# Performance work log

Hardware: AMD Instinct MI355X
Metric: run time of the kernel (lower is better)

The kernel has to match this reference:

```python
import jax, jax.numpy as jnp
import numpy as np

B, N, C = 2, 2048, 1024
H, D = 16, 64  # n_q_heads, head_dim
EPS = 1e-6


def setup_inputs() -> dict:
    key = jax.random.key(0)
    ks = jax.random.split(key, 6)
    x = jax.random.normal(ks[0], (B, N, C), dtype=jnp.float32)
    context = jax.random.normal(ks[1], (B, N, C), dtype=jnp.float32)
    # realistic RoPE tables, rotary_dim = head_dim (non-interleaved GLM-style)
    inv_freq = 1.0 / (10000.0 ** (np.arange(0, D, 2, dtype=np.float32) / D))
    ang = np.arange(N, dtype=np.float32)[:, None] * inv_freq[None, :]  # [N, D/2]
    ang = np.concatenate([ang, ang], axis=-1)  # [N, D]
    cos = jnp.broadcast_to(jnp.cos(ang)[None], (B, N, D)).astype(jnp.float32)
    sin = jnp.broadcast_to(jnp.sin(ang)[None], (B, N, D)).astype(jnp.float32)
    s = 1.0 / np.sqrt(C)
    Wq = jax.random.normal(ks[2], (2 * C, C), dtype=jnp.float32) * s
    Wkv = jax.random.normal(ks[3], (2 * C, C), dtype=jnp.float32) * s
    Wo = jax.random.normal(ks[4], (C, C), dtype=jnp.float32) * s
    bo = jnp.zeros((C,), dtype=jnp.float32)
    q_norm_w = jnp.ones((D,), dtype=jnp.float32)
    k_norm_w = jnp.ones((D,), dtype=jnp.float32)
    return {"x": x, "context": context, "cos": cos, "sin": sin,
            "Wq": Wq, "Wkv": Wkv, "Wo": Wo, "bo": bo,
            "q_norm_w": q_norm_w, "k_norm_w": k_norm_w}


def _zm_rmsnorm(t, w):
    # zero-mean RMSNorm over last (head_dim) axis: LayerNorm without bias
    t = t - jnp.mean(t, axis=-1, keepdims=True)
    var = jnp.mean(t * t, axis=-1, keepdims=True)
    return t * jax.lax.rsqrt(var + EPS) * w


def _rotate_half(t):
    t1, t2 = jnp.split(t, 2, axis=-1)
    return jnp.concatenate([-t2, t1], axis=-1)


def reference(x, context, cos, sin, Wq, Wkv, Wo, bo, q_norm_w, k_norm_w):
    b, n1, c = x.shape
    n2 = context.shape[1]
    # fused q+gate projection: [b, n1, 2*C] -> [b, n1, H, 2D], per-head chunk
    qg = (x @ Wq.T).reshape(b, n1, H, 2 * D)
    q = qg[..., :D]                      # [b, n1, H, D]
    gate = qg[..., D:].reshape(b, n1, H * D)  # [b, n1, C]
    q = _zm_rmsnorm(q, q_norm_w).transpose(0, 2, 1, 3)  # [b, H, n1, D]
    # fused k+v projection: [b, n2, 2*C] -> [b, n2, H, 2D]
    kv = (context @ Wkv.T).reshape(b, n2, H, 2 * D)
    k = _zm_rmsnorm(kv[..., :D], k_norm_w).transpose(0, 2, 1, 3)  # [b, H, n2, D]
    v = kv[..., D:].transpose(0, 2, 1, 3)                         # [b, H, n2, D]
    # RoPE (full head_dim rotary)
    cos_b = cos[:, None]  # [b, 1, n, D]
    sin_b = sin[:, None]
    q = q * cos_b + _rotate_half(q) * sin_b
    k = k * cos_b + _rotate_half(k) * sin_b
    # SDPA (non-causal cross attention)
    scale = D ** -0.5
    scores = jnp.einsum('bhqd,bhkd->bhqk', q, k) * scale
    attn = jax.nn.softmax(scores, axis=-1)
    attn_out = jnp.einsum('bhqk,bhkd->bhqd', attn, v)
    attn_out = attn_out.transpose(0, 2, 1, 3).reshape(b, n1, H * D)  # [b, n1, C]
    # gated output combine + out projection
    attn_out = attn_out * jax.nn.sigmoid(gate)
    return attn_out @ Wo.T + bo
```

## Files before the change

### kernel.cpp

```cpp
#include <hip/hip_runtime.h>
#include <cstdint>
#include <cstddef>


#define B_ 2
#define N_ 2048
#define C_ 1024
#define H_ 16
#define D_ 64
#define K_ 1024
#define PK_ 2048
#define EPS_ 1e-6f
#define LOG2E_ 1.44269504088896f
#define SMAX_ 12.0f

typedef __bf16 b16x8 __attribute__((ext_vector_type(8)));
typedef float f32x4 __attribute__((ext_vector_type(4)));

__device__ __forceinline__ unsigned short f2bf(float f) {
  union { float f; unsigned u; } a; a.f = f;
  unsigned r = a.u + 0x7FFFu + ((a.u >> 16) & 1u);
  return (unsigned short)(r >> 16);
}
__device__ __forceinline__ float bf2f(unsigned short u) {
  union { unsigned u; float f; } a; a.u = ((unsigned)u) << 16; return a.f;
}

__device__ __forceinline__ void cast_one(const float* __restrict__ src,
                                         unsigned short* __restrict__ dst, int e) {
  float4 v = *(const float4*)(src + e);
  *(ushort4*)(dst + e) = make_ushort4(f2bf(v.x), f2bf(v.y), f2bf(v.z), f2bf(v.w));
}

__device__ __forceinline__ void pack_one(const float* __restrict__ src,
                                         unsigned short* __restrict__ dst, int e) {
  float4 v = *(const float4*)(src + e);
  const int r = e >> 10, k = e & 1023;
  unsigned short* p = dst + ((size_t)r << 11) + ((k >> 5) << 6) + (k & 31);
  const unsigned short h0 = f2bf(v.x), h1 = f2bf(v.y), h2 = f2bf(v.z), h3 = f2bf(v.w);
  *(ushort4*)p = make_ushort4(h0, h1, h2, h3);
  *(ushort4*)(p + 32) = make_ushort4(f2bf(v.x - bf2f(h0)), f2bf(v.y - bf2f(h1)),
                                     f2bf(v.z - bf2f(h2)), f2bf(v.w - bf2f(h3)));
}

__global__ __launch_bounds__(256) void pack_all(
    const float* __restrict__ x, const float* __restrict__ Wq,
    const float* __restrict__ ctx, const float* __restrict__ Wkv,
    const float* __restrict__ Wo,
    unsigned short* __restrict__ xb, unsigned short* __restrict__ wqb,
    unsigned short* __restrict__ cb, unsigned short* __restrict__ wkvb,
    unsigned short* __restrict__ wop)
{
  const int e = (blockIdx.x * 256 + threadIdx.x) << 2;
  if (e < 4194304)       cast_one(x,   xb,  e);
  else if (e < 6291456)  cast_one(Wq,  wqb, e - 4194304);
  else if (e < 10485760) cast_one(ctx, cb,  e - 6291456);
  else if (e < 12582912) cast_one(Wkv, wkvb, e - 10485760);
  else                   pack_one(Wo,  wop, e - 12582912);
}

__global__ __launch_bounds__(256) void gemm_qkv(
    const unsigned short* __restrict__ xb, const unsigned short* __restrict__ wqb,
    const unsigned short* __restrict__ cb, const unsigned short* __restrict__ wkvb,
    const float* __restrict__ cosb, const float* __restrict__ sinb,
    const float* __restrict__ qnw, const float* __restrict__ knw,
    unsigned short* __restrict__ Qbo, unsigned short* __restrict__ Kbo,
    unsigned short* __restrict__ gate, unsigned short* __restrict__ vt, float qscale)
{
  __shared__ __align__(16) unsigned short As[128 * 64];
  __shared__ __align__(16) unsigned short Bs[128 * 64];
  const int tid = threadIdx.x, lane = tid & 63, wave = tid >> 6;

  const int id = blockIdx.x;
  const int swz = (id & 7) * 128 + (id >> 3);
  const bool isQ = swz < 512;
  const int local = swz & 511;
  const int bm = (local >> 4) << 7, bn = (local & 15) << 7;
  const int wm = (wave >> 1) << 6, wn = (wave & 1) << 6;

  const unsigned short* Ap = isQ ? xb : cb;
  const unsigned short* Bp = isQ ? wqb : wkvb;

  const int srow = lane >> 3;
  const int sslot = (lane & 7) ^ srow;
  const size_t rbytes = (size_t)K_ * 2;
  const char* aSrc = (const char*)Ap + (size_t)(bm + srow) * rbytes + (sslot << 4);
  const char* bSrc = (const char*)Bp + (size_t)(bn + srow) * rbytes + (sslot << 4);

  f32x4 acc[4][4];
  #pragma unroll
  for (int i = 0; i < 4; ++i)
    #pragma unroll
    for (int j = 0; j < 4; ++j) acc[i][j] = (f32x4){0.f, 0.f, 0.f, 0.f};

  const int fr = lane & 15, fs = lane >> 4;

  for (int ks = 0; ks < K_ / 64; ++ks) {
    const size_t ko = (size_t)ks << 7;
    #pragma unroll
    for (int i = 0; i < 4; ++i) {
      const int g = (wave << 2) + i;
      __builtin_amdgcn_global_load_lds(
          (const __attribute__((address_space(1))) void*)(aSrc + (size_t)(g << 3) * rbytes + ko),
          (__attribute__((address_space(3))) void*)((char*)As + (g << 10)), 16, 0, 0);
      __builtin_amdgcn_global_load_lds(
          (const __attribute__((address_space(1))) void*)(bSrc + (size_t)(g << 3) * rbytes + ko),
          (__attribute__((address_space(3))) void*)((char*)Bs + (g << 10)), 16, 0, 0);
    }
    __syncthreads();

    b16x8 a[4][2], b[4][2];
    #pragma unroll
    for (int t = 0; t < 4; ++t) {
      const int ar = wm + (t << 4) + fr;
      const char* pa = (const char*)As + (ar << 7);
      a[t][0] = *(const b16x8*)(pa + ((fs ^ (ar & 7)) << 4));
      a[t][1] = *(const b16x8*)(pa + (((4 + fs) ^ (ar & 7)) << 4));
      const int br = wn + (t << 4) + fr;
      const char* pb = (const char*)Bs + (br << 7);
      b[t][0] = *(const b16x8*)(pb + ((fs ^ (br & 7)) << 4));
      b[t][1] = *(const b16x8*)(pb + (((4 + fs) ^ (br & 7)) << 4));
    }
    #pragma unroll
    for (int mi = 0; mi < 4; ++mi)
      #pragma unroll
      for (int ni = 0; ni < 4; ++ni) {
        acc[mi][ni] = __builtin_amdgcn_mfma_f32_16x16x32_bf16(a[mi][0], b[ni][0], acc[mi][ni], 0, 0, 0);
        acc[mi][ni] = __builtin_amdgcn_mfma_f32_16x16x32_bf16(a[mi][1], b[ni][1], acc[mi][ni], 0, 0, 0);
      }
    __syncthreads();
  }

  const int g = lane >> 4;
  const int h = bn >> 7;
  if (wn == 0) {
    const float* nw = isQ ? qnw : knw;
    const float oscale = isQ ? qscale : 1.0f;
    unsigned short* nOut = isQ ? Qbo : Kbo;
    float wv[4];
    #pragma unroll
    for (int ni = 0; ni < 4; ++ni) wv[ni] = nw[(ni << 4) + fr];
    #pragma unroll
    for (int mi = 0; mi < 4; ++mi) {
      #pragma unroll
      for (int r = 0; r < 4; ++r) {
        const int t = bm + wm + (mi << 4) + (g << 2) + r;
        float v0 = acc[mi][0][r], v1 = acc[mi][1][r];
        float v2 = acc[mi][2][r], v3 = acc[mi][3][r];
        float s = (v0 + v1) + (v2 + v3);
        #pragma unroll
        for (int off = 1; off < 16; off <<= 1) s += __shfl_xor(s, off);
        const float mean = s * (1.f / 64.f);
        v0 -= mean; v1 -= mean; v2 -= mean; v3 -= mean;
        float s2 = (v0*v0 + v1*v1) + (v2*v2 + v3*v3);
        #pragma unroll
        for (int off = 1; off < 16; off <<= 1) s2 += __shfl_xor(s2, off);
        const float rq = rsqrtf(s2 * (1.f / 64.f) + EPS_);
        const float x0 = v0 * rq * wv[0], x1 = v1 * rq * wv[1];
        const float x2 = v2 * rq * wv[2], x3 = v3 * rq * wv[3];
        const float* cr = cosb + (size_t)t * 64;
        const float* sr = sinb + (size_t)t * 64;
        const float o0 = x0 * cr[fr]    - x2 * sr[fr];
        const float o1 = x1 * cr[16+fr] - x3 * sr[16+fr];
        const float o2 = x2 * cr[32+fr] + x0 * sr[32+fr];
        const float o3 = x3 * cr[48+fr] + x1 * sr[48+fr];
        unsigned short* dp = nOut + (((size_t)((t >> 11) * H_ + h)) * N_ + (t & 2047)) * 64;
        dp[fr]      = f2bf(o0 * oscale);
        dp[16 + fr] = f2bf(o1 * oscale);
        dp[32 + fr] = f2bf(o2 * oscale);
        dp[48 + fr] = f2bf(o3 * oscale);
      }
    }
  } else if (isQ) {
    #pragma unroll
    for (int mi = 0; mi < 4; ++mi)
      #pragma unroll
      for (int r = 0; r < 4; ++r) {
        const int t = bm + wm + (mi << 4) + (g << 2) + r;
        unsigned short* gp = gate + (size_t)t * C_ + h * 64;
        #pragma unroll
        for (int ni = 0; ni < 4; ++ni) gp[(ni << 4) + fr] = f2bf(acc[mi][ni][r]);
      }
  } else {
    #pragma unroll
    for (int mi = 0; mi < 4; ++mi) {
      const int t0 = bm + wm + (mi << 4) + (g << 2);
      const int bb = t0 >> 11, n0 = t0 & 2047;
      #pragma unroll
      for (int ni = 0; ni < 4; ++ni) {
        const int dv = (ni << 4) + fr;
        ushort4 pk = make_ushort4(f2bf(acc[mi][ni][0]), f2bf(acc[mi][ni][1]),
                                  f2bf(acc[mi][ni][2]), f2bf(acc[mi][ni][3]));
        *(ushort4*)(vt + ((size_t)(bb * H_ + h) * 64 + dv) * N_ + n0) = pk;
      }
    }
  }
}

__global__ __launch_bounds__(256) void gemm_nt_hilo(
    const unsigned short* __restrict__ Ap, const unsigned short* __restrict__ Bp,
    float* __restrict__ Cm, int M, int N, const float* __restrict__ bias)
{
  __shared__ __align__(16) unsigned short As[128 * 64];
  __shared__ __align__(16) unsigned short Bs[64 * 64];
  const int tid = threadIdx.x, lane = tid & 63, wave = tid >> 6;

  const int nwg = gridDim.x, id = blockIdx.x;
  const int swz = (id & 7) * (nwg >> 3) + (id >> 3);
  const int nbn = N >> 6;
  const int bm = (swz / nbn) << 7, bn = (swz % nbn) << 6;
  const int wm = (wave >> 1) << 6, wn = (wave & 1) << 5;

  const int srow = lane >> 3;
  const int sslot = (lane & 7) ^ srow;
  const size_t rbytes = (size_t)K_ * 4;
  const char* aSrc = (const char*)Ap + (size_t)(bm + srow) * rbytes + (sslot << 4);
  const char* bSrc = (const char*)Bp + (size_t)(bn + srow) * rbytes + (sslot << 4);

  f32x4 acc[4][2];
  #pragma unroll
  for (int i = 0; i < 4; ++i)
    #pragma unroll
    for (int j = 0; j < 2; ++j) acc[i][j] = (f32x4){0.f, 0.f, 0.f, 0.f};

  const int fr = lane & 15, fs = lane >> 4;
  const int hoff = (fs ^ (fr & 7)) << 4;

  for (int ks = 0; ks < K_ / 32; ++ks) {
    const size_t ko = (size_t)ks << 7;
    #pragma unroll
    for (int i = 0; i < 4; ++i) {
      const int ga = (wave << 2) + i;
      __builtin_amdgcn_global_load_lds(
          (const __attribute__((address_space(1))) void*)(aSrc + (size_t)(ga << 3) * rbytes + ko),
          (__attribute__((address_space(3))) void*)((char*)As + (ga << 10)), 16, 0, 0);
    }
    #pragma unroll
    for (int i = 0; i < 2; ++i) {
      const int gb = (wave << 1) + i;
      __builtin_amdgcn_global_load_lds(
          (const __attribute__((address_space(1))) void*)(bSrc + (size_t)(gb << 3) * rbytes + ko),
          (__attribute__((address_space(3))) void*)((char*)Bs + (gb << 10)), 16, 0, 0);
    }
    __syncthreads();

    b16x8 ah[4], al[4], bh[2], bl[2];
    #pragma unroll
    for (int t = 0; t < 4; ++t) {
      const char* pa = (const char*)As + ((wm + (t << 4) + fr) << 7);
      ah[t] = *(const b16x8*)(pa + hoff);
      al[t] = *(const b16x8*)(pa + (hoff ^ 64));
    }
    #pragma unroll
    for (int t = 0; t < 2; ++t) {
      const char* pb = (const char*)Bs + ((wn + (t << 4) + fr) << 7);
      bh[t] = *(const b16x8*)(pb + hoff);
      bl[t] = *(const b16x8*)(pb + (hoff ^ 64));
    }
    #pragma unroll
    for (int mi = 0; mi < 4; ++mi)
      #pragma unroll
      for (int ni = 0; ni < 2; ++ni) {
        acc[mi][ni] = __builtin_amdgcn_mfma_f32_16x16x32_bf16(ah[mi], bh[ni], acc[mi][ni], 0, 0, 0);
        acc[mi][ni] = __builtin_amdgcn_mfma_f32_16x16x32_bf16(al[mi], bh[ni], acc[mi][ni], 0, 0, 0);
        acc[mi][ni] = __builtin_amdgcn_mfma_f32_16x16x32_bf16(ah[mi], bl[ni], acc[mi][ni], 0, 0, 0);
      }
    __syncthreads();
  }

  const int rbase = (lane >> 4) << 2;
  #pragma unroll
  for (int mi = 0; mi < 4; ++mi)
    #pragma unroll
    for (int ni = 0; ni < 2; ++ni) {
      const int n = bn + wn + (ni << 4) + fr;
      const float badd = bias ? bias[n] : 0.f;
      #pragma unroll
      for (int r = 0; r < 4; ++r) {
        const int m = bm + wm + (mi << 4) + rbase + r;
        Cm[(size_t)m * N + n] = acc[mi][ni][r] + badd;
      }
    }
}

__global__ __launch_bounds__(256) void flash_bf16(
    const unsigned short* __restrict__ Qb, const unsigned short* __restrict__ Kb,
    const unsigned short* __restrict__ Vt, const unsigned short* __restrict__ gateb,
    unsigned short* __restrict__ gp)
{
  const int id = blockIdx.x;
  const int swzb = (id & 7) * 64 + (id >> 3);
  const int q0 = (swzb & 15) * 128;
  const int h = (swzb >> 4) & 15;
  const int b = swzb >> 8;
  const int tid = threadIdx.x, lane = tid & 63, wave = tid >> 6;
  __shared__ __align__(16) unsigned short Ks[2][64 * 64];
  __shared__ __align__(16) unsigned short Vss[2][64 * 64];
  __shared__ __align__(16) __bf16 Ps[4][2][16][72];
  const int bh = b * H_ + h;
  const int g = lane >> 4, fr = lane & 15;

  b16x8 qA0, qA1, qB0, qB1;
  {
    const unsigned short* QrowA = Qb + ((size_t)bh * N_ + q0 + wave*32 + fr) * D_;
    qA0 = *(const b16x8*)(QrowA + (g << 3));
    qA1 = *(const b16x8*)(QrowA + 32 + (g << 3));
    qB0 = *(const b16x8*)(QrowA + 16 * D_ + (g << 3));
    qB1 = *(const b16x8*)(QrowA + 16 * D_ + 32 + (g << 3));
  }

  f32x4 oA[4], oB[4];
  #pragma unroll
  for (int r = 0; r < 4; ++r) {
    oA[r] = (f32x4){0.f, 0.f, 0.f, 0.f};
    oB[r] = (f32x4){0.f, 0.f, 0.f, 0.f};
  }
  float lA = 0.f, lB = 0.f;

  const unsigned short* Kbh  = Kb + (size_t)bh * N_ * D_;
  const unsigned short* Vtbh = Vt + (size_t)bh * D_ * N_;
  const int swzK = ((lane & 7) ^ (lane >> 3)) << 4;
  __bf16* PwA = &Ps[wave][0][0][0] + fr * 72;
  __bf16* PwB = &Ps[wave][1][0][0] + fr * 72;

  #define STAGE(buf, j0)                                                          \
    {                                                                             \
      _Pragma("unroll")                                                           \
      for (int i = 0; i < 2; ++i) {                                               \
        const int gg = wave * 2 + i;                                              \
        const char* ksrc = (const char*)(Kbh + (size_t)((j0) + gg * 8) * D_) +    \
                           (lane >> 3) * 128 + swzK;                              \
        __builtin_amdgcn_global_load_lds(                                         \
            (const __attribute__((address_space(1))) void*)ksrc,                  \
            (__attribute__((address_space(3))) void*)((char*)Ks[buf] + gg * 1024),\
            16, 0, 0);                                                            \
        const int dv = gg * 8 + (lane >> 3);                                      \
        const char* vsrc = (const char*)(Vtbh + (size_t)dv * N_ + (j0)) + swzK;   \
        __builtin_amdgcn_global_load_lds(                                         \
            (const __attribute__((address_space(1))) void*)vsrc,                  \
            (__attribute__((address_space(3))) void*)((char*)Vss[buf] + gg * 1024),\
            16, 0, 0);                                                            \
      }                                                                           \
    }

  STAGE(0, 0);
  int cur = 0;
  for (int j0 = 0; j0 < N_; j0 += 64) {
    __syncthreads();
    if (j0 + 64 < N_) STAGE(cur ^ 1, j0 + 64);

    const unsigned short* Kbuf = Ks[cur];
    const unsigned short* Vbuf = Vss[cur];
    const int cb0 = g << 4;
    __builtin_amdgcn_s_setprio(1);
    #pragma unroll
    for (int t = 0; t < 4; ++t) {
      const int krow = t * 16 + fr;
      const char* kbp = (const char*)Kbuf + krow * 128;
      const int f = (krow & 7) << 4;
      b16x8 kf0 = *(const b16x8*)(kbp + (cb0 ^ f));
      b16x8 kf1 = *(const b16x8*)(kbp + ((64 + cb0) ^ f));
      f32x4 sA = __builtin_amdgcn_mfma_f32_16x16x32_bf16(kf0, qA0, (f32x4){0.f,0.f,0.f,0.f}, 0, 0, 0);
      sA = __builtin_amdgcn_mfma_f32_16x16x32_bf16(kf1, qA1, sA, 0, 0, 0);
      f32x4 sB = __builtin_amdgcn_mfma_f32_16x16x32_bf16(kf0, qB0, (f32x4){0.f,0.f,0.f,0.f}, 0, 0, 0);
      sB = __builtin_amdgcn_mfma_f32_16x16x32_bf16(kf1, qB1, sB, 0, 0, 0);
      union { __bf16 hb[4]; ushort4 u4; } pkA, pkB;
      #pragma unroll
      for (int r = 0; r < 4; ++r) {
        const float pA = __builtin_amdgcn_exp2f(sA[r] - SMAX_);
        lA += pA;
        pkA.hb[r] = (__bf16)pA;
        const float pB = __builtin_amdgcn_exp2f(sB[r] - SMAX_);
        lB += pB;
        pkB.hb[r] = (__bf16)pB;
      }
      *(ushort4*)(PwA + t * 16 + (g << 2)) = pkA.u4;
      *(ushort4*)(PwB + t * 16 + (g << 2)) = pkB.u4;
    }
    __builtin_amdgcn_s_setprio(0);

    b16x8 pfA[2], pfB[2];
    #pragma unroll
    for (int c = 0; c < 2; ++c) {
      pfA[c] = *(const b16x8*)(PwA + c * 32 + (g << 3));
      pfB[c] = *(const b16x8*)(PwB + c * 32 + (g << 3));
    }

    __builtin_amdgcn_s_setprio(1);
    #pragma unroll
    for (int dt = 0; dt < 4; ++dt) {
      const int vrow = dt * 16 + fr;
      const char* vbp = (const char*)Vbuf + vrow * 128;
      const int fv = (vrow & 7) << 4;
      #pragma unroll
      for (int c = 0; c < 2; ++c) {
        b16x8 vf = *(const b16x8*)(vbp + ((c * 64 + cb0) ^ fv));
        oA[dt] = __builtin_amdgcn_mfma_f32_16x16x32_bf16(pfA[c], vf, oA[dt], 0, 0, 0);
        oB[dt] = __builtin_amdgcn_mfma_f32_16x16x32_bf16(pfB[c], vf, oB[dt], 0, 0, 0);
      }
    }
    __builtin_amdgcn_s_setprio(0);
    cur ^= 1;
  }
  #undef STAGE

  lA += __shfl_xor(lA, 16); lA += __shfl_xor(lA, 32);
  lB += __shfl_xor(lB, 16); lB += __shfl_xor(lB, 32);

  #pragma unroll
  for (int r = 0; r < 4; ++r) {
    const float lqA = __shfl(lA, (g << 2) + r);
    const float lqB = __shfl(lB, (g << 2) + r);
    #pragma unroll
    for (int set = 0; set < 2; ++set) {
      const float inv = 1.f / (set ? lqB : lqA);
      const int q = q0 + wave * 32 + set * 16 + (g << 2) + r;
      const size_t qa = (size_t)(b * N_ + q);
      #pragma unroll
      for (int dt = 0; dt < 4; ++dt) {
        const int d = (dt << 4) + fr;
        const float o = (set ? oB[dt][r] : oA[dt][r]) * inv;
        const float gate = bf2f(gateb[qa * C_ + h * 64 + d]);
        const float sg = 1.f / (1.f + __expf(-gate));
        const float val = o * sg;
        const int k = h * 64 + d;
        unsigned short* p = gp + qa * PK_ + ((k >> 5) << 6) + (k & 31);
        const unsigned short hi = f2bf(val);
        p[0]  = hi;
        p[32] = f2bf(val - bf2f(hi));
      }
    }
  }
}

extern "C" void kernel_launch(void* const* d_in, const int* in_sizes, int n_in,
                              void* d_out, int out_size, void* d_ws, size_t ws_size,
                              hipStream_t stream) {
  const float* x    = (const float*)d_in[0];
  const float* ctx  = (const float*)d_in[1];
  const float* cosb = (const float*)d_in[2];
  const float* sinb = (const float*)d_in[3];
  const float* Wq   = (const float*)d_in[4];
  const float* Wkv  = (const float*)d_in[5];
  const float* Wo   = (const float*)d_in[6];
  const float* bo   = (const float*)d_in[7];
  const float* qnw  = (const float*)d_in[8];
  const float* knw  = (const float*)d_in[9];
  float* out = (float*)d_out;

  char* ws = (char*)d_ws;
  unsigned short* Qb   = (unsigned short*)(ws);
  unsigned short* Kb   = (unsigned short*)(ws + (size_t)8388608);
  unsigned short* Vt   = (unsigned short*)(ws + (size_t)16777216);
  unsigned short* gate = (unsigned short*)(ws + (size_t)25165824);
  unsigned short* gpk  = (unsigned short*)(ws + (size_t)41943040);
  unsigned short* xb   = (unsigned short*)(ws + (size_t)58720256);
  unsigned short* cb   = (unsigned short*)(ws + (size_t)67108864);
  unsigned short* wqb  = (unsigned short*)(ws + (size_t)75497472);
  unsigned short* wkvb = (unsigned short*)(ws + (size_t)79691776);
  unsigned short* wop  = (unsigned short*)(ws + (size_t)83886080);

  pack_all<<<dim3(13312), dim3(256), 0, stream>>>(x, Wq, ctx, Wkv, Wo, xb, wqb, cb, wkvb, wop);
  gemm_qkv<<<dim3(1024), dim3(256), 0, stream>>>(xb, wqb, cb, wkvb, cosb, sinb, qnw, knw,
                                                 Qb, Kb, gate, Vt, 0.125f * LOG2E_);
  flash_bf16<<<dim3(512), dim3(256), 0, stream>>>(Qb, Kb, Vt, gate, gpk);
  gemm_nt_hilo<<<dim3(512), dim3(256), 0, stream>>>(gpk, wop, out, 4096, 1024, bo);
}
```

Measured before the change: 156.6 us.

## Enlarge QKV GEMM tiles to 256x256 with double-buffered LDS staging

The fused Q/gate and K/V projection GEMM now uses 256x256 block tiles with 8 waves per block instead of 128x128 tiles with 4 waves. The grid shrinks from 1024 to 256 blocks. The k-loop double-buffers the async global-to-LDS copies, so the next k-slice is fetched while MFMAs run on the current one. It also raises wave priority during the MFMA phase. The aim is more operand reuse per LDS load and hidden global load latency. In exchange it uses 128KB of LDS per block and 128 accumulator registers per thread, which risks spills or low occupancy, and one block per CU may leave little room to hide tail effects.

Result: faster. 150.4 us (-4.0%).

```diff
diff --git a/kernel.cpp b/kernel.cpp
--- a/kernel.cpp
+++ b/kernel.cpp
@@ -59,7 +59,7 @@
   else                   pack_one(Wo,  wop, e - 12582912);
 }
 
-__global__ __launch_bounds__(256) void gemm_qkv(
+__global__ __launch_bounds__(512, 2) void gemm_qkv(
     const unsigned short* __restrict__ xb, const unsigned short* __restrict__ wqb,
     const unsigned short* __restrict__ cb, const unsigned short* __restrict__ wkvb,
     const float* __restrict__ cosb, const float* __restrict__ sinb,
@@ -67,16 +67,16 @@
     unsigned short* __restrict__ Qbo, unsigned short* __restrict__ Kbo,
     unsigned short* __restrict__ gate, unsigned short* __restrict__ vt, float qscale)
 {
-  __shared__ __align__(16) unsigned short As[128 * 64];
-  __shared__ __align__(16) unsigned short Bs[128 * 64];
+  __shared__ __align__(16) unsigned short As[2][256 * 64];
+  __shared__ __align__(16) unsigned short Bs[2][256 * 64];
   const int tid = threadIdx.x, lane = tid & 63, wave = tid >> 6;
 
   const int id = blockIdx.x;
-  const int swz = (id & 7) * 128 + (id >> 3);
-  const bool isQ = swz < 512;
-  const int local = swz & 511;
-  const int bm = (local >> 4) << 7, bn = (local & 15) << 7;
-  const int wm = (wave >> 1) << 6, wn = (wave & 1) << 6;
+  const int swz = (id & 7) * 32 + (id >> 3);
+  const bool isQ = swz < 128;
+  const int local = swz & 127;
+  const int bm = (local >> 3) << 8, bn = (local & 7) << 8;
+  const int wm = (wave >> 2) << 7, wn = (wave & 3) << 6;
 
   const unsigned short* Ap = isQ ? xb : cb;
   const unsigned short* Bp = isQ ? wqb : wkvb;
@@ -87,53 +87,68 @@
   const char* aSrc = (const char*)Ap + (size_t)(bm + srow) * rbytes + (sslot << 4);
   const char* bSrc = (const char*)Bp + (size_t)(bn + srow) * rbytes + (sslot << 4);
 
-  f32x4 acc[4][4];
+  f32x4 acc[8][4];
   #pragma unroll
-  for (int i = 0; i < 4; ++i)
+  for (int i = 0; i < 8; ++i)
     #pragma unroll
     for (int j = 0; j < 4; ++j) acc[i][j] = (f32x4){0.f, 0.f, 0.f, 0.f};
 
   const int fr = lane & 15, fs = lane >> 4;
 
-  for (int ks = 0; ks < K_ / 64; ++ks) {
-    const size_t ko = (size_t)ks << 7;
-    #pragma unroll
-    for (int i = 0; i < 4; ++i) {
-      const int g = (wave << 2) + i;
-      __builtin_amdgcn_global_load_lds(
-          (const __attribute__((address_space(1))) void*)(aSrc + (size_t)(g << 3) * rbytes + ko),
-          (__attribute__((address_space(3))) void*)((char*)As + (g << 10)), 16, 0, 0);
-      __builtin_amdgcn_global_load_lds(
-          (const __attribute__((address_space(1))) void*)(bSrc + (size_t)(g << 3) * rbytes + ko),
-          (__attribute__((address_space(3))) void*)((char*)Bs + (g << 10)), 16, 0, 0);
-    }
+  #define QSTAGE(buf, kt)                                                          \
+    {                                                                              \
+      const size_t ko = (size_t)(kt) << 7;                                         \
+      _Pragma("unroll")                                                            \
+      for (int i = 0; i < 4; ++i) {                                                \
+        const int g = (wave << 2) + i;                                             \
+        __builtin_amdgcn_global_load_lds(                                          \
+            (const __attribute__((address_space(1))) void*)(aSrc + (size_t)(g << 3) * rbytes + ko), \
+            (__attribute__((address_space(3))) void*)((char*)As[buf] + (g << 10)), \
+            16, 0, 0);                                                             \
+        __builtin_amdgcn_global_load_lds(                                          \
+            (const __attribute__((address_space(1))) void*)(bSrc + (size_t)(g << 3) * rbytes + ko), \
+            (__attribute__((address_space(3))) void*)((char*)Bs[buf] + (g << 10)), \
+            16, 0, 0);                                                             \
+      }                                                                            \
+    }
+
+  QSTAGE(0, 0);
+  int cur = 0;
+  for (int kt = 0; kt < 16; ++kt) {
     __syncthreads();
-
-    b16x8 a[4][2], b[4][2];
-    #pragma unroll
-    for (int t = 0; t < 4; ++t) {
-      const int ar = wm + (t << 4) + fr;
-      const char* pa = (const char*)As + (ar << 7);
-      a[t][0] = *(const b16x8*)(pa + ((fs ^ (ar & 7)) << 4));
-      a[t][1] = *(const b16x8*)(pa + (((4 + fs) ^ (ar & 7)) << 4));
-      const int br = wn + (t << 4) + fr;
-      const char* pb = (const char*)Bs + (br << 7);
-      b[t][0] = *(const b16x8*)(pb + ((fs ^ (br & 7)) << 4));
-      b[t][1] = *(const b16x8*)(pb + (((4 + fs) ^ (br & 7)) << 4));
-    }
-    #pragma unroll
-    for (int mi = 0; mi < 4; ++mi)
+    if (kt + 1 < 16) QSTAGE(cur ^ 1, kt + 1);
+
+    const char* Abuf = (const char*)As[cur];
+    const char* Bbuf = (const char*)Bs[cur];
+    __builtin_amdgcn_s_setprio(1);
+    #pragma unroll
+    for (int kk = 0; kk < 2; ++kk) {
+      b16x8 a[8], b[4];
+      #pragma unroll
+      for (int mi = 0; mi < 8; ++mi) {
+        const int ar = wm + (mi << 4) + fr;
+        a[mi] = *(const b16x8*)(Abuf + (ar << 7) + ((((kk << 2) + fs) ^ (ar & 7)) << 4));
+      }
       #pragma unroll
       for (int ni = 0; ni < 4; ++ni) {
-        acc[mi][ni] = __builtin_amdgcn_mfma_f32_16x16x32_bf16(a[mi][0], b[ni][0], acc[mi][ni], 0, 0, 0);
-        acc[mi][ni] = __builtin_amdgcn_mfma_f32_16x16x32_bf16(a[mi][1], b[ni][1], acc[mi][ni], 0, 0, 0);
-      }
-    __syncthreads();
-  }
+        const int br = wn + (ni << 4) + fr;
+        b[ni] = *(const b16x8*)(Bbuf + (br << 7) + ((((kk << 2) + fs) ^ (br & 7)) << 4));
+      }
+      #pragma unroll
+      for (int mi = 0; mi < 8; ++mi)
+        #pragma unroll
+        for (int ni = 0; ni < 4; ++ni)
+          acc[mi][ni] = __builtin_amdgcn_mfma_f32_16x16x32_bf16(a[mi], b[ni], acc[mi][ni], 0, 0, 0);
+    }
+    __builtin_amdgcn_s_setprio(0);
+    cur ^= 1;
+  }
+  #undef QSTAGE
 
   const int g = lane >> 4;
-  const int h = bn >> 7;
-  if (wn == 0) {
+  const int h = (bn >> 7) + (wn >> 7);
+  const bool normHalf = ((wn >> 6) & 1) == 0;
+  if (normHalf) {
     const float* nw = isQ ? qnw : knw;
     const float oscale = isQ ? qscale : 1.0f;
     unsigned short* nOut = isQ ? Qbo : Kbo;
@@ -141,7 +156,7 @@
     #pragma unroll
     for (int ni = 0; ni < 4; ++ni) wv[ni] = nw[(ni << 4) + fr];
     #pragma unroll
-    for (int mi = 0; mi < 4; ++mi) {
+    for (int mi = 0; mi < 8; ++mi) {
       #pragma unroll
       for (int r = 0; r < 4; ++r) {
         const int t = bm + wm + (mi << 4) + (g << 2) + r;
@@ -173,7 +188,7 @@
     }
   } else if (isQ) {
     #pragma unroll
-    for (int mi = 0; mi < 4; ++mi)
+    for (int mi = 0; mi < 8; ++mi)
       #pragma unroll
       for (int r = 0; r < 4; ++r) {
         const int t = bm + wm + (mi << 4) + (g << 2) + r;
@@ -183,7 +198,7 @@
       }
   } else {
     #pragma unroll
-    for (int mi = 0; mi < 4; ++mi) {
+    for (int mi = 0; mi < 8; ++mi) {
       const int t0 = bm + wm + (mi << 4) + (g << 2);
       const int bb = t0 >> 11, n0 = t0 & 2047;
       #pragma unroll
@@ -461,8 +476,8 @@
   unsigned short* wop  = (unsigned short*)(ws + (size_t)83886080);
 
   pack_all<<<dim3(13312), dim3(256), 0, stream>>>(x, Wq, ctx, Wkv, Wo, xb, wqb, cb, wkvb, wop);
-  gemm_qkv<<<dim3(1024), dim3(256), 0, stream>>>(xb, wqb, cb, wkvb, cosb, sinb, qnw, knw,
-                                                 Qb, Kb, gate, Vt, 0.125f * LOG2E_);
+  gemm_qkv<<<dim3(256), dim3(512), 0, stream>>>(xb, wqb, cb, wkvb, cosb, sinb, qnw, knw,
+                                                Qb, Kb, gate, Vt, 0.125f * LOG2E_);
   flash_bf16<<<dim3(512), dim3(256), 0, stream>>>(Qb, Kb, Vt, gate, gpk);
   gemm_nt_hilo<<<dim3(512), dim3(256), 0, stream>>>(gpk, wop, out, 4096, 1024, bo);
 }
```
